# Performance work log

Hardware: AMD Instinct MI355X
Metric: run time of the kernel (lower is better)

Reference implementation:

```python
import jax, jax.numpy as jnp
import numpy as np

D_MODEL = 1024
NUM_HEADS = 16
NUM_KV_HEADS = 4
D_K = D_MODEL // NUM_HEADS          # 64
GROUP = NUM_HEADS // NUM_KV_HEADS   # 4
D_KV = D_MODEL // GROUP             # 256


def setup_inputs() -> dict:
    key = jax.random.key(0)
    ks = jax.random.split(key, 12)
    B, S = 2, 2048
    sc = 0.02
    return {
        "query": jax.random.normal(ks[0], (B, S, D_MODEL), jnp.float32),
        "key": jax.random.normal(ks[1], (B, S, D_MODEL), jnp.float32),
        "value": jax.random.normal(ks[2], (B, S, D_MODEL), jnp.float32),
        "w_q": jax.random.normal(ks[3], (D_MODEL, D_MODEL), jnp.float32) * sc,
        "b_q": jnp.zeros((D_MODEL,), jnp.float32),
        "w_k": jax.random.normal(ks[4], (D_KV, D_MODEL), jnp.float32) * sc,
        "b_k": jnp.zeros((D_KV,), jnp.float32),
        "w_v": jax.random.normal(ks[5], (D_KV, D_MODEL), jnp.float32) * sc,
        "b_v": jnp.zeros((D_KV,), jnp.float32),
        "w_o": jax.random.normal(ks[6], (D_MODEL, D_MODEL), jnp.float32) * sc,
        "b_o": jnp.zeros((D_MODEL,), jnp.float32),
    }


def reference(query, key, value, w_q, b_q, w_k, b_k, w_v, b_v, w_o, b_o):
    B, S, _ = query.shape
    # projections (torch Linear: x @ W.T + b)
    Q = query @ w_q.T + b_q            # [B,S,d_model]
    K = key @ w_k.T + b_k              # [B,S,d_kv]
    V = value @ w_v.T + b_v            # [B,S,d_kv]
    # [B, Hkv, G, S, Dk] for Q; [B, Hkv, S, Dk] for K/V.
    # repeat_interleave(group, dim=1) on K/V == sharing each KV head across
    # its group of query heads, so we contract without duplicating K/V.
    Q = Q.reshape(B, S, NUM_KV_HEADS, GROUP, D_K).transpose(0, 2, 3, 1, 4)
    K = K.reshape(B, S, NUM_KV_HEADS, D_K).transpose(0, 2, 1, 3)
    V = V.reshape(B, S, NUM_KV_HEADS, D_K).transpose(0, 2, 1, 3)
    scale = 1.0 / jnp.sqrt(jnp.asarray(D_K, Q.dtype))
    scores = jnp.einsum('bhgsd,bhtd->bhgst', Q, K) * scale  # [B,Hkv,G,S,S]
    attn = jax.nn.softmax(scores, axis=-1)
    out = jnp.einsum('bhgst,bhtd->bhgsd', attn, V)          # [B,Hkv,G,S,Dk]
    # -> [B,S,Hkv*G*Dk] = [B,S,d_model]
    out = out.transpose(0, 3, 1, 2, 4).reshape(B, S, D_MODEL)
    return out @ w_o.T + b_o
```

## Files before the change

### kernel.cpp

```cpp
#include <hip/hip_runtime.h>
#include <hip/hip_bf16.h>
#include <stdint.h>

typedef unsigned short u16;
typedef unsigned int   u32;
typedef short s16x8 __attribute__((ext_vector_type(8)));
typedef u16   u16x4 __attribute__((ext_vector_type(4)));
typedef u16   u16x8 __attribute__((ext_vector_type(8)));
typedef u32   u32x2 __attribute__((ext_vector_type(2)));
typedef u32   u32x4 __attribute__((ext_vector_type(4)));
typedef float f32x4  __attribute__((ext_vector_type(4)));
typedef float f32x16 __attribute__((ext_vector_type(16)));
typedef float f4     __attribute__((ext_vector_type(4)));

#define MFMA(a,b,c)   __builtin_amdgcn_mfma_f32_16x16x32_bf16((a),(b),(c),0,0,0)
#define MFMA32(a,b,c) __builtin_amdgcn_mfma_f32_32x32x16_bf16((a),(b),(c),0,0,0)

__device__ __forceinline__ u16 f2b(float f){
  union { float f; unsigned u; } v; v.f = f;
  unsigned r = v.u + 0x7fffu + ((v.u >> 16) & 1u);
  return (u16)(r >> 16);
}

__device__ __forceinline__ u32 cvtpk(float lo, float hi){
  u32 r;
  asm("v_cvt_pk_bf16_f32 %0, %1, %2" : "=v"(r) : "v"(lo), "v"(hi));
  return r;
}

__device__ __forceinline__ float exp2h(float x){
  float r;
  asm("v_exp_f32 %0, %1" : "=v"(r) : "v"(x));
  return r;
}

__device__ __forceinline__ void gll16(const void* g, void* l){
  __builtin_amdgcn_global_load_lds(
      (const __attribute__((address_space(1))) void*)g,
      (__attribute__((address_space(3))) void*)l, 16, 0, 0);
}

__global__ __launch_bounds__(256) void wcast(const float* __restrict__ wq,
                                             const float* __restrict__ wk,
                                             const float* __restrict__ wv,
                                             const float* __restrict__ wo,
                                             u16* dq, u16* dk, u16* dv, u16* dov){
  int e = (blockIdx.x * 256 + threadIdx.x) * 4;
  const float* s; u16* d; int off;
  if      (e < 1048576){ s = wq; d = dq;  off = 0; }
  else if (e < 1310720){ s = wk; d = dk;  off = 1048576; }
  else if (e < 1572864){ s = wv; d = dv;  off = 1310720; }
  else                 { s = wo; d = dov; off = 1572864; }
  int i = e - off;
  f4 v = *(const f4*)(s + i);
  u32x2 o; o[0] = cvtpk(v[0], v[1]); o[1] = cvtpk(v[2], v[3]);
  *(u32x2*)(d + i) = o;
}

__global__ __launch_bounds__(256) void qkv_gemm(
    const float* __restrict__ qa, const float* __restrict__ ka, const float* __restrict__ va,
    const u16* __restrict__ wq, const u16* __restrict__ wk, const u16* __restrict__ wv,
    const float* __restrict__ bq, const float* __restrict__ bk, const float* __restrict__ bv,
    u16* Qo, u16* Ko, u16* Vto){
  __shared__ u16 As[2][64*32];
  __shared__ u16 Bs[2][128*32];
  const int tid = threadIdx.x, lane = tid & 63, wid = tid >> 6;
  const int lb = (blockIdx.x & 7) * 96 + (blockIdx.x >> 3);
  const float* A; const u16* B; const float* bias; int N; float cscale; int bm, bn;
  bool isV = false;
  if (lb < 512)      { A=qa; B=wq; bias=bq; N=1024; cscale=0.18033688011112f; bm=lb>>3;         bn=lb&7; }
  else if (lb < 640) { A=ka; B=wk; bias=bk; N=256;  cscale=1.0f;              bm=(lb-512)>>1;   bn=(lb-512)&1; }
  else               { A=va; B=wv; bias=bv; N=256;  cscale=1.0f;              bm=(lb-640)>>1;   bn=(lb-640)&1; isV = true; }
  const int wr = wid >> 1, wc = wid & 1;
  const int r15 = lane & 15, kg = lane >> 4;

  const u16*  Bg = B + (size_t)bn * 128 * 1024;
  const float* Ag = A + (size_t)bm * 64 * 1024;
  f32x4 acc[2][4] = {};

  const int arow = tid >> 2, ac8 = (tid & 3) << 3;

  #pragma unroll
  for (int i = 0; i < 2; i++){
    int cc = wid + i*4, row = cc*16 + (lane >> 2);
    gll16((const char*)Bg + ((size_t)row*1024)*2 + (lane & 3)*16, (char*)&Bs[0][0] + cc*1024);
  }
  {
    f4 v0 = *(const f4*)(Ag + (size_t)arow*1024 + ac8);
    f4 v1 = *(const f4*)(Ag + (size_t)arow*1024 + ac8 + 4);
    u32x4 o; o[0]=cvtpk(v0[0],v0[1]); o[1]=cvtpk(v0[2],v0[3]);
             o[2]=cvtpk(v1[0],v1[1]); o[3]=cvtpk(v1[2],v1[3]);
    *(u32x4*)&As[0][arow*32 + ac8] = o;
  }
  __syncthreads();

  for (int k0 = 0; k0 < 1024; k0 += 32){
    const int cur = (k0 >> 5) & 1;
    const bool pf = (k0 + 32) < 1024;
    f4 a0, a1;
    if (pf){
      #pragma unroll
      for (int i = 0; i < 2; i++){
        int cc = wid + i*4, row = cc*16 + (lane >> 2);
        gll16((const char*)Bg + ((size_t)row*1024 + k0 + 32)*2 + (lane & 3)*16,
              (char*)&Bs[cur^1][0] + cc*1024);
      }
      a0 = *(const f4*)(Ag + (size_t)arow*1024 + k0 + 32 + ac8);
      a1 = *(const f4*)(Ag + (size_t)arow*1024 + k0 + 32 + ac8 + 4);
    }
    s16x8 af[2], bf[4];
    #pragma unroll
    for (int i = 0; i < 2; i++)
      af[i] = *(const s16x8*)&As[cur][(wr*32 + i*16 + r15)*32 + kg*8];
    #pragma unroll
    for (int j = 0; j < 4; j++)
      bf[j] = *(const s16x8*)&Bs[cur][(wc*64 + j*16 + r15)*32 + kg*8];
    __builtin_amdgcn_s_setprio(1);
    #pragma unroll
    for (int i = 0; i < 2; i++)
      #pragma unroll
      for (int j = 0; j < 4; j++)
        acc[i][j] = MFMA(af[i], bf[j], acc[i][j]);
    __builtin_amdgcn_s_setprio(0);
    if (pf){
      u32x4 o; o[0]=cvtpk(a0[0],a0[1]); o[1]=cvtpk(a0[2],a0[3]);
               o[2]=cvtpk(a1[0],a1[1]); o[3]=cvtpk(a1[2],a1[3]);
      *(u32x4*)&As[cur^1][arow*32 + ac8] = o;
    }
    __syncthreads();
  }

  if (isV){
    #pragma unroll
    for (int i = 0; i < 2; i++){
      int row0 = bm*64 + wr*32 + i*16 + kg*4;
      int bb = row0 >> 11, t = row0 & 2047;
      #pragma unroll
      for (int j = 0; j < 4; j++){
        int col = bn*128 + wc*64 + j*16 + r15;
        float bj = bias[col];
        u16x4 vv;
        #pragma unroll
        for (int r = 0; r < 4; r++) vv[r] = f2b(acc[i][j][r] + bj);
        *(u16x4*)&Vto[((size_t)(bb*256 + col) << 11) + t] = vv;
      }
    }
  } else {
    u16* C = (lb < 512) ? Qo : Ko;
    #pragma unroll
    for (int i = 0; i < 2; i++){
      int row = bm*64 + wr*32 + i*16 + kg*4;
      #pragma unroll
      for (int j = 0; j < 4; j++){
        int col = bn*128 + wc*64 + j*16 + r15;
        float bj = bias[col];
        #pragma unroll
        for (int r = 0; r < 4; r++)
          C[(size_t)(row + r)*N + col] = f2b((acc[i][j][r] + bj) * cscale);
      }
    }
  }
}

__global__ __launch_bounds__(256) void gemm_o(const u16* __restrict__ Aw,
                                              const u16* __restrict__ Bw,
                                              const float* __restrict__ bias,
                                              float* __restrict__ Cv){
  __shared__ u16 As[2][128*32];
  __shared__ u16 Bs[2][128*32];
  const int tid = threadIdx.x, lane = tid & 63, wid = tid >> 6;
  const int lb = (blockIdx.x & 7) * 32 + (blockIdx.x >> 3);
  const int bm = lb >> 3, bn = lb & 7;
  const int wr = wid >> 1, wc = wid & 1;
  const int r15 = lane & 15, kg = lane >> 4;
  const u16* Ag = Aw + (size_t)bm * 128 * 1024;
  const u16* Bg = Bw + (size_t)bn * 128 * 1024;
  f32x4 acc[4][4] = {};

  auto stage = [&](int buf, int k0){
    #pragma unroll
    for (int i = 0; i < 2; i++){
      int cc = wid + i*4, row = cc*16 + (lane >> 2);
      gll16((const char*)Ag + ((size_t)row*1024 + k0)*2 + (lane & 3)*16, (char*)&As[buf][0] + cc*1024);
      gll16((const char*)Bg + ((size_t)row*1024 + k0)*2 + (lane & 3)*16, (char*)&Bs[buf][0] + cc*1024);
    }
  };
  stage(0, 0);
  __syncthreads();
  for (int k0 = 0; k0 < 1024; k0 += 32){
    const int cur = (k0 >> 5) & 1;
    if (k0 + 32 < 1024) stage(cur ^ 1, k0 + 32);
    s16x8 af[4], bf[4];
    #pragma unroll
    for (int i = 0; i < 4; i++)
      af[i] = *(const s16x8*)&As[cur][(wr*64 + i*16 + r15)*32 + kg*8];
    #pragma unroll
    for (int j = 0; j < 4; j++)
      bf[j] = *(const s16x8*)&Bs[cur][(wc*64 + j*16 + r15)*32 + kg*8];
    __builtin_amdgcn_s_setprio(1);
    #pragma unroll
    for (int i = 0; i < 4; i++)
      #pragma unroll
      for (int j = 0; j < 4; j++)
        acc[i][j] = MFMA(af[i], bf[j], acc[i][j]);
    __builtin_amdgcn_s_setprio(0);
    __syncthreads();
  }
  #pragma unroll
  for (int i = 0; i < 4; i++){
    int row = bm*128 + wr*64 + i*16 + kg*4;
    #pragma unroll
    for (int j = 0; j < 4; j++){
      int col = bn*128 + wc*64 + j*16 + r15;
      float bj = bias[col];
      #pragma unroll
      for (int r = 0; r < 4; r++)
        Cv[(size_t)(row + r)*1024 + col] = acc[i][j][r] + bj;
    }
  }
}

__global__ __launch_bounds__(512, 4) void attn_fwd(const u16* __restrict__ Qp,
                                                   const u16* __restrict__ Kp,
                                                   const u16* __restrict__ Vt,
                                                   u16* __restrict__ Op){
  __shared__ u16 Ks[2][2][64*64];
  __shared__ u16 Vs[2][2][64*64];
  const int tid = threadIdx.x, lane = tid & 63, w = tid >> 6;
  const int wg = w & 3, g = w >> 2;
  const int bx = blockIdx.x;
  const int qt = bx & 15, h = (bx >> 4) & 15, b = bx >> 8;
  const int kvh = h >> 2;
  const int l31 = lane & 31, hh = lane >> 5;
  const int srow = lane >> 3;
  const int scol16 = ((lane & 7) ^ srow) << 4;

  const size_t qrow0 = (size_t)(b*2048 + qt*128 + wg*32 + l31) << 10;
  s16x8 qf[4];
  #pragma unroll
  for (int db = 0; db < 4; db++)
    qf[db] = *(const s16x8*)(Qp + qrow0 + h*64 + db*16 + hh*8);

  f32x16 oacc[2] = {};
  const f32x16 ZERO = {};
  float lsum = 0.f;

  auto stage = [&](int buf, int t0){
    #pragma unroll
    for (int i = 0; i < 2; i++){
      int cc = wg + i*4;
      int row = cc*8 + srow;
      const u16* ksrc = Kp + ((size_t)(b*2048 + t0 + row) << 8) + kvh*64;
      gll16((const char*)ksrc + scol16, (char*)&Ks[g][buf][0] + cc*1024);
      const u16* vsrc = Vt + ((size_t)((b*4 + kvh)*64 + row) << 11) + t0;
      gll16((const char*)vsrc + scol16, (char*)&Vs[g][buf][0] + cc*1024);
    }
  };

  stage(0, g*64);
  __syncthreads();

  for (int it = 0; it < 16; it++){
    const int cur = it & 1;
    if (it + 1 < 16) stage(cur ^ 1, (2*(it + 1) + g)*64);

    f32x16 sacc[2];
    __builtin_amdgcn_s_setprio(1);
    #pragma unroll
    for (int kb2 = 0; kb2 < 2; kb2++){
      #pragma unroll
      for (int db = 0; db < 4; db++){
        int row = kb2*32 + l31;
        int slot = (db*2 + hh) ^ (row & 7);
        s16x8 kf = *(const s16x8*)((const char*)&Ks[g][cur][0] + row*128 + slot*16);
        sacc[kb2] = MFMA32(kf, qf[db], (db == 0) ? ZERO : sacc[kb2]);
      }
    }
    __builtin_amdgcn_s_setprio(0);

    u32 W[2][4][2];
    #pragma unroll
    for (int kb2 = 0; kb2 < 2; kb2++){
      float p[16];
      #pragma unroll
      for (int r = 0; r < 16; r++){
        p[r] = exp2h(sacc[kb2][r]);
        lsum += p[r];
      }
      #pragma unroll
      for (int a = 0; a < 4; a++){
        W[kb2][a][0] = cvtpk(p[4*a + 0], p[4*a + 1]);
        W[kb2][a][1] = cvtpk(p[4*a + 2], p[4*a + 3]);
      }
    }

    s16x8 pa[4];
    #pragma unroll
    for (int kq = 0; kq < 4; kq++){
      const int kb2 = kq >> 1, c = kq & 1;
      u32x4 dw;
      #pragma unroll
      for (int pp = 0; pp < 2; pp++){
        u32 x = W[kb2][2*c][pp], y = W[kb2][2*c + 1][pp];
        asm volatile("v_permlane32_swap_b32 %0, %1" : "+v"(x), "+v"(y));
        dw[pp] = x; dw[2 + pp] = y;
      }
      pa[kq] = *(const s16x8*)&dw;
    }

    __builtin_amdgcn_s_setprio(1);
    #pragma unroll
    for (int dblk = 0; dblk < 2; dblk++){
      #pragma unroll
      for (int kq = 0; kq < 4; kq++){
        int row = dblk*32 + l31;
        int slot = (kq*2 + hh) ^ (row & 7);
        s16x8 vf = *(const s16x8*)((const char*)&Vs[g][cur][0] + row*128 + slot*16);
        oacc[dblk] = MFMA32(pa[kq], vf, oacc[dblk]);
      }
    }
    __builtin_amdgcn_s_setprio(0);
    __syncthreads();
  }

  float rsum = lsum + __shfl_xor(lsum, 32, 64);
  float* Om = (float*)&Ks[0][0][0];
  float* Ls = (float*)&Vs[0][0][0];
  if (g == 1){
    #pragma unroll
    for (int reg = 0; reg < 16; reg++){
      int q = (reg & 3) + 4*hh + 8*(reg >> 2);
      #pragma unroll
      for (int dblk = 0; dblk < 2; dblk++)
        Om[(wg*32 + q)*64 + dblk*32 + l31] = oacc[dblk][reg];
    }
    if (hh == 0) Ls[wg*32 + l31] = rsum;
  }
  __syncthreads();
  if (g == 0){
    rsum += Ls[wg*32 + l31];
    float rinv = __builtin_amdgcn_rcpf(rsum);
    const size_t obase = (size_t)(b*2048 + qt*128 + wg*32) << 10;
    #pragma unroll
    for (int reg = 0; reg < 16; reg++){
      const int qrow = (reg & 3) + 4*hh + 8*(reg >> 2);
      float rq = __shfl(rinv, qrow, 64);
      #pragma unroll
      for (int dblk = 0; dblk < 2; dblk++){
        float v = (oacc[dblk][reg] + Om[(wg*32 + qrow)*64 + dblk*32 + l31]) * rq;
        Op[obase + ((size_t)qrow << 10) + h*64 + dblk*32 + l31] = f2b(v);
      }
    }
  }
}

extern "C" void kernel_launch(void* const* d_in, const int* in_sizes, int n_in,
                              void* d_out, int out_size, void* d_ws, size_t ws_size,
                              hipStream_t stream){
  const float* query = (const float*)d_in[0];
  const float* key   = (const float*)d_in[1];
  const float* value = (const float*)d_in[2];
  const float* w_q   = (const float*)d_in[3];
  const float* b_q   = (const float*)d_in[4];
  const float* w_k   = (const float*)d_in[5];
  const float* b_k   = (const float*)d_in[6];
  const float* w_v   = (const float*)d_in[7];
  const float* b_v   = (const float*)d_in[8];
  const float* w_o   = (const float*)d_in[9];
  const float* b_o   = (const float*)d_in[10];

  char* ws = (char*)d_ws;
  size_t off = 0;
  u16* wqb = (u16*)(ws + off); off += (size_t)1024*1024*2;
  u16* wkb = (u16*)(ws + off); off += (size_t)256*1024*2;
  u16* wvb = (u16*)(ws + off); off += (size_t)256*1024*2;
  u16* wob = (u16*)(ws + off); off += (size_t)1024*1024*2;
  u16* Qw  = (u16*)(ws + off); off += (size_t)4096*1024*2;
  u16* Kw  = (u16*)(ws + off); off += (size_t)4096*256*2;
  u16* Vtw = (u16*)(ws + off); off += (size_t)4096*256*2;
  u16* AOw = (u16*)(ws + off); off += (size_t)4096*1024*2;

  wcast<<<2560, 256, 0, stream>>>(w_q, w_k, w_v, w_o, wqb, wkb, wvb, wob);

  qkv_gemm<<<768, 256, 0, stream>>>(query, key, value, wqb, wkb, wvb,
                                    b_q, b_k, b_v, Qw, Kw, Vtw);

  attn_fwd<<<512, 512, 0, stream>>>(Qw, Kw, Vtw, AOw);

  gemm_o<<<256, 256, 0, stream>>>(AOw, wob, b_o, (float*)d_out);
}
```

Baseline: 102.6 us.

## Triple-buffer GEMMs with async LDS loads, swizzling, and fine-grained vmcnt waits

qkv_gemm now loads fp32 activations straight into LDS with global_load_lds instead of through registers, and converts them to bf16 when reading the fragments. Both GEMMs use a 3-stage ring buffer with XOR-swizzled LDS layouts, explicit s_waitcnt vmcnt counts and raw barriers in place of __syncthreads. gemm_o moves to 64x128 tiles and 512 blocks for better occupancy. attn_fwd waits only on the older prefetch before its barrier. The aim is to hide global load latency and cut LDS bank conflicts, at the cost of more LDS and correctness that depends on hand-counted vmcnt values.

```diff
diff --git a/kernel.cpp b/kernel.cpp
--- a/kernel.cpp
+++ b/kernel.cpp
@@ -15,6 +15,9 @@
 
 #define MFMA(a,b,c)   __builtin_amdgcn_mfma_f32_16x16x32_bf16((a),(b),(c),0,0,0)
 #define MFMA32(a,b,c) __builtin_amdgcn_mfma_f32_32x32x16_bf16((a),(b),(c),0,0,0)
+
+#define BAR()   __builtin_amdgcn_s_barrier()
+#define SCHED() __builtin_amdgcn_sched_barrier(0)
 
 __device__ __forceinline__ u16 f2b(float f){
   union { float f; unsigned u; } v; v.f = f;
@@ -62,59 +65,54 @@
     const u16* __restrict__ wq, const u16* __restrict__ wk, const u16* __restrict__ wv,
     const float* __restrict__ bq, const float* __restrict__ bk, const float* __restrict__ bv,
     u16* Qo, u16* Ko, u16* Vto){
-  __shared__ u16 As[2][64*32];
-  __shared__ u16 Bs[2][128*32];
+  __shared__ float Asf[3][64*32];
+  __shared__ u16   Bsw[3][128*32];
   const int tid = threadIdx.x, lane = tid & 63, wid = tid >> 6;
   const int lb = (blockIdx.x & 7) * 96 + (blockIdx.x >> 3);
   const float* A; const u16* B; const float* bias; int N; float cscale; int bm, bn;
   bool isV = false;
-  if (lb < 512)      { A=qa; B=wq; bias=bq; N=1024; cscale=0.18033688011112f; bm=lb>>3;         bn=lb&7; }
-  else if (lb < 640) { A=ka; B=wk; bias=bk; N=256;  cscale=1.0f;              bm=(lb-512)>>1;   bn=(lb-512)&1; }
-  else               { A=va; B=wv; bias=bv; N=256;  cscale=1.0f;              bm=(lb-640)>>1;   bn=(lb-640)&1; isV = true; }
+  if (lb < 512)      { A=qa; B=wq; bias=bq; N=1024; cscale=0.18033688011112f; bm=lb>>3;       bn=lb&7; }
+  else if (lb < 640) { A=ka; B=wk; bias=bk; N=256;  cscale=1.0f;              bm=(lb-512)>>1; bn=(lb-512)&1; }
+  else               { A=va; B=wv; bias=bv; N=256;  cscale=1.0f;              bm=(lb-640)>>1; bn=(lb-640)&1; isV = true; }
   const int wr = wid >> 1, wc = wid & 1;
   const int r15 = lane & 15, kg = lane >> 4;
 
-  const u16*  Bg = B + (size_t)bn * 128 * 1024;
+  const u16*   Bg = B + (size_t)bn * 128 * 1024;
   const float* Ag = A + (size_t)bm * 64 * 1024;
   f32x4 acc[2][4] = {};
 
-  const int arow = tid >> 2, ac8 = (tid & 3) << 3;
-
-  #pragma unroll
-  for (int i = 0; i < 2; i++){
-    int cc = wid + i*4, row = cc*16 + (lane >> 2);
-    gll16((const char*)Bg + ((size_t)row*1024)*2 + (lane & 3)*16, (char*)&Bs[0][0] + cc*1024);
-  }
-  {
-    f4 v0 = *(const f4*)(Ag + (size_t)arow*1024 + ac8);
-    f4 v1 = *(const f4*)(Ag + (size_t)arow*1024 + ac8 + 4);
-    u32x4 o; o[0]=cvtpk(v0[0],v0[1]); o[1]=cvtpk(v0[2],v0[3]);
-             o[2]=cvtpk(v1[0],v1[1]); o[3]=cvtpk(v1[2],v1[3]);
-    *(u32x4*)&As[0][arow*32 + ac8] = o;
-  }
-  __syncthreads();
-
-  for (int k0 = 0; k0 < 1024; k0 += 32){
-    const int cur = (k0 >> 5) & 1;
-    const bool pf = (k0 + 32) < 1024;
-    f4 a0, a1;
-    if (pf){
-      #pragma unroll
-      for (int i = 0; i < 2; i++){
-        int cc = wid + i*4, row = cc*16 + (lane >> 2);
-        gll16((const char*)Bg + ((size_t)row*1024 + k0 + 32)*2 + (lane & 3)*16,
-              (char*)&Bs[cur^1][0] + cc*1024);
-      }
-      a0 = *(const f4*)(Ag + (size_t)arow*1024 + k0 + 32 + ac8);
-      a1 = *(const f4*)(Ag + (size_t)arow*1024 + k0 + 32 + ac8 + 4);
-    }
+  auto stage = [&](int buf, int k0){
+    #pragma unroll
+    for (int i = 0; i < 2; i++){
+      int cc = wid + i*4;
+      int brow = cc*16 + (lane >> 2);
+      int bslot = (lane & 3) ^ ((brow >> 1) & 3);
+      gll16((const char*)Bg + (size_t)brow*2048 + k0*2 + bslot*16,
+            (char*)&Bsw[buf][0] + cc*1024);
+      int arow = cc*8 + (lane >> 3);
+      int aslot = (lane & 7) ^ (arow & 7);
+      gll16((const char*)Ag + (size_t)arow*4096 + k0*4 + aslot*16,
+            (char*)&Asf[buf][0] + cc*1024);
+    }
+  };
+
+  auto compute = [&](int buf){
     s16x8 af[2], bf[4];
     #pragma unroll
-    for (int i = 0; i < 2; i++)
-      af[i] = *(const s16x8*)&As[cur][(wr*32 + i*16 + r15)*32 + kg*8];
-    #pragma unroll
-    for (int j = 0; j < 4; j++)
-      bf[j] = *(const s16x8*)&Bs[cur][(wc*64 + j*16 + r15)*32 + kg*8];
+    for (int i = 0; i < 2; i++){
+      int row = wr*32 + i*16 + r15;
+      const char* rb = (const char*)&Asf[buf][0] + row*128;
+      f4 va_ = *(const f4*)(rb + ((((kg*2)    ) ^ (row & 7)) << 4));
+      f4 vb_ = *(const f4*)(rb + ((((kg*2) + 1) ^ (row & 7)) << 4));
+      u32x4 o; o[0]=cvtpk(va_[0],va_[1]); o[1]=cvtpk(va_[2],va_[3]);
+               o[2]=cvtpk(vb_[0],vb_[1]); o[3]=cvtpk(vb_[2],vb_[3]);
+      af[i] = *(const s16x8*)&o;
+    }
+    #pragma unroll
+    for (int j = 0; j < 4; j++){
+      int row = wc*64 + j*16 + r15;
+      bf[j] = *(const s16x8*)((const char*)&Bsw[buf][0] + row*64 + ((kg ^ ((row >> 1) & 3)) << 4));
+    }
     __builtin_amdgcn_s_setprio(1);
     #pragma unroll
     for (int i = 0; i < 2; i++)
@@ -122,13 +120,29 @@
       for (int j = 0; j < 4; j++)
         acc[i][j] = MFMA(af[i], bf[j], acc[i][j]);
     __builtin_amdgcn_s_setprio(0);
-    if (pf){
-      u32x4 o; o[0]=cvtpk(a0[0],a0[1]); o[1]=cvtpk(a0[2],a0[3]);
-               o[2]=cvtpk(a1[0],a1[1]); o[3]=cvtpk(a1[2],a1[3]);
-      *(u32x4*)&As[cur^1][arow*32 + ac8] = o;
-    }
-    __syncthreads();
-  }
+  };
+
+  stage(0, 0); stage(1, 32); stage(2, 64);
+  int bsel = 0;
+  for (int t = 0; t < 29; t++){
+    asm volatile("s_waitcnt vmcnt(8)" ::: "memory");
+    BAR(); SCHED();
+    compute(bsel);
+    SCHED(); BAR();
+    stage(bsel, (t + 3)*32);
+    bsel = (bsel == 2) ? 0 : bsel + 1;
+  }
+  asm volatile("s_waitcnt vmcnt(8)" ::: "memory");
+  BAR(); SCHED();
+  compute(bsel);
+  bsel = (bsel == 2) ? 0 : bsel + 1;
+  asm volatile("s_waitcnt vmcnt(4)" ::: "memory");
+  BAR(); SCHED();
+  compute(bsel);
+  bsel = (bsel == 2) ? 0 : bsel + 1;
+  asm volatile("s_waitcnt vmcnt(0)" ::: "memory");
+  BAR(); SCHED();
+  compute(bsel);
 
   if (isV){
     #pragma unroll
@@ -166,49 +180,78 @@
                                               const u16* __restrict__ Bw,
                                               const float* __restrict__ bias,
                                               float* __restrict__ Cv){
-  __shared__ u16 As[2][128*32];
-  __shared__ u16 Bs[2][128*32];
+  __shared__ u16 As[3][64*32];
+  __shared__ u16 Bs[3][128*32];
   const int tid = threadIdx.x, lane = tid & 63, wid = tid >> 6;
-  const int lb = (blockIdx.x & 7) * 32 + (blockIdx.x >> 3);
+  const int lb = (blockIdx.x & 7) * 64 + (blockIdx.x >> 3);
   const int bm = lb >> 3, bn = lb & 7;
   const int wr = wid >> 1, wc = wid & 1;
   const int r15 = lane & 15, kg = lane >> 4;
-  const u16* Ag = Aw + (size_t)bm * 128 * 1024;
+  const u16* Ag = Aw + (size_t)bm * 64 * 1024;
   const u16* Bg = Bw + (size_t)bn * 128 * 1024;
-  f32x4 acc[4][4] = {};
+  f32x4 acc[2][4] = {};
 
   auto stage = [&](int buf, int k0){
-    #pragma unroll
-    for (int i = 0; i < 2; i++){
-      int cc = wid + i*4, row = cc*16 + (lane >> 2);
-      gll16((const char*)Ag + ((size_t)row*1024 + k0)*2 + (lane & 3)*16, (char*)&As[buf][0] + cc*1024);
-      gll16((const char*)Bg + ((size_t)row*1024 + k0)*2 + (lane & 3)*16, (char*)&Bs[buf][0] + cc*1024);
+    int arow = wid*16 + (lane >> 2);
+    int aslot = (lane & 3) ^ ((arow >> 1) & 3);
+    gll16((const char*)Ag + (size_t)arow*2048 + k0*2 + aslot*16,
+          (char*)&As[buf][0] + wid*1024);
+    #pragma unroll
+    for (int i = 0; i < 2; i++){
+      int cc = wid + i*4;
+      int brow = cc*16 + (lane >> 2);
+      int bslot = (lane & 3) ^ ((brow >> 1) & 3);
+      gll16((const char*)Bg + (size_t)brow*2048 + k0*2 + bslot*16,
+            (char*)&Bs[buf][0] + cc*1024);
     }
   };
-  stage(0, 0);
-  __syncthreads();
-  for (int k0 = 0; k0 < 1024; k0 += 32){
-    const int cur = (k0 >> 5) & 1;
-    if (k0 + 32 < 1024) stage(cur ^ 1, k0 + 32);
-    s16x8 af[4], bf[4];
-    #pragma unroll
-    for (int i = 0; i < 4; i++)
-      af[i] = *(const s16x8*)&As[cur][(wr*64 + i*16 + r15)*32 + kg*8];
-    #pragma unroll
-    for (int j = 0; j < 4; j++)
-      bf[j] = *(const s16x8*)&Bs[cur][(wc*64 + j*16 + r15)*32 + kg*8];
+
+  auto compute = [&](int buf){
+    s16x8 af[2], bf[4];
+    #pragma unroll
+    for (int i = 0; i < 2; i++){
+      int row = wr*32 + i*16 + r15;
+      af[i] = *(const s16x8*)((const char*)&As[buf][0] + row*64 + ((kg ^ ((row >> 1) & 3)) << 4));
+    }
+    #pragma unroll
+    for (int j = 0; j < 4; j++){
+      int row = wc*64 + j*16 + r15;
+      bf[j] = *(const s16x8*)((const char*)&Bs[buf][0] + row*64 + ((kg ^ ((row >> 1) & 3)) << 4));
+    }
     __builtin_amdgcn_s_setprio(1);
     #pragma unroll
-    for (int i = 0; i < 4; i++)
+    for (int i = 0; i < 2; i++)
       #pragma unroll
       for (int j = 0; j < 4; j++)
         acc[i][j] = MFMA(af[i], bf[j], acc[i][j]);
     __builtin_amdgcn_s_setprio(0);
-    __syncthreads();
-  }
+  };
+
+  stage(0, 0); stage(1, 32); stage(2, 64);
+  int bsel = 0;
+  for (int t = 0; t < 29; t++){
+    asm volatile("s_waitcnt vmcnt(6)" ::: "memory");
+    BAR(); SCHED();
+    compute(bsel);
+    SCHED(); BAR();
+    stage(bsel, (t + 3)*32);
+    bsel = (bsel == 2) ? 0 : bsel + 1;
+  }
+  asm volatile("s_waitcnt vmcnt(6)" ::: "memory");
+  BAR(); SCHED();
+  compute(bsel);
+  bsel = (bsel == 2) ? 0 : bsel + 1;
+  asm volatile("s_waitcnt vmcnt(3)" ::: "memory");
+  BAR(); SCHED();
+  compute(bsel);
+  bsel = (bsel == 2) ? 0 : bsel + 1;
+  asm volatile("s_waitcnt vmcnt(0)" ::: "memory");
+  BAR(); SCHED();
+  compute(bsel);
+
   #pragma unroll
-  for (int i = 0; i < 4; i++){
-    int row = bm*128 + wr*64 + i*16 + kg*4;
+  for (int i = 0; i < 2; i++){
+    int row = bm*64 + wr*32 + i*16 + kg*4;
     #pragma unroll
     for (int j = 0; j < 4; j++){
       int col = bn*128 + wc*64 + j*16 + r15;
@@ -258,11 +301,16 @@
   };
 
   stage(0, g*64);
-  __syncthreads();
 
   for (int it = 0; it < 16; it++){
     const int cur = it & 1;
-    if (it + 1 < 16) stage(cur ^ 1, (2*(it + 1) + g)*64);
+    if (it + 1 < 16){
+      stage(cur ^ 1, (2*(it + 1) + g)*64);
+      asm volatile("s_waitcnt vmcnt(4)" ::: "memory");
+    } else {
+      asm volatile("s_waitcnt vmcnt(0)" ::: "memory");
+    }
+    BAR(); SCHED();
 
     f32x16 sacc[2];
     __builtin_amdgcn_s_setprio(1);
@@ -320,8 +368,9 @@
       }
     }
     __builtin_amdgcn_s_setprio(0);
-    __syncthreads();
-  }
+    SCHED(); BAR();
+  }
+  __syncthreads();
 
   float rsum = lsum + __shfl_xor(lsum, 32, 64);
   float* Om = (float*)&Ks[0][0][0];
@@ -387,5 +436,5 @@
 
   attn_fwd<<<512, 512, 0, stream>>>(Qw, Kw, Vtw, AOw);
 
-  gemm_o<<<256, 256, 0, stream>>>(AOw, wob, b_o, (float*)d_out);
-}
+  gemm_o<<<512, 256, 0, stream>>>(AOw, wob, b_o, (float*)d_out);
+}
```

Result: faster. 97.75 us (-4.8%).
